# Kernel tuning notes

Measured on AMD Instinct MI355X. Metric: run time of the kernel, lower is better.

The kernel has to match this reference:

```python
import jax, jax.numpy as jnp
import numpy as np

TEMPERATURE = 0.1
NUM_CLASSES = 21
L2_EPS = 1e-12   # torch F.normalize eps
NEG = -1e9       # masking value for invalid (absent-class) logit slots


def setup_inputs() -> dict:
    key = jax.random.key(0)
    k1, k2 = jax.random.split(key)
    features = jax.random.normal(k1, (16, 512, 64, 64), dtype=jnp.float32)
    labels = jax.random.randint(k2, (16, 513, 513), 0, NUM_CLASSES, dtype=jnp.int32)
    return {"features": features, "labels": labels}


def reference(features, labels):
    B, D, H, W = features.shape
    C = NUM_CLASSES
    # torch: F.interpolate(labels.float()[:,None], (H,W), mode='bilinear').squeeze(1).long()
    lab = jax.image.resize(labels.astype(jnp.float32)[:, None], (B, 1, H, W),
                           method="bilinear", antialias=False)
    lab = lab[:, 0].astype(jnp.int32)                     # [B,H,W]

    # per-image, per-class masked feature pooling (segment reduce)
    masks = (lab[:, None, :, :] == jnp.arange(C)[None, :, None, None]).astype(features.dtype)  # [B,C,H,W]
    sums = jnp.einsum('bdhw,bchw->bcd', features, masks)  # [B,C,D]
    norms = jnp.linalg.norm(sums, axis=-1, keepdims=True)
    protos = sums / jnp.maximum(norms, L2_EPS)            # normalized prototypes [B,C,D]
    pres = masks.sum((2, 3)) > 0                          # [B,C] class present in image

    # all pairwise prototype dots: S[c,e,i,j] = <proto[i,c], proto[j,e]> / T
    S = jnp.einsum('icd,jed->ceij', protos, protos) / TEMPERATURE  # [C,C,B,B]
    presT = pres.T                                        # [C,B]
    valid = presT[:, None, :, None] & presT[None, :, None, :]       # [C,C,B,B]
    masked = jnp.where(valid, S, NEG)

    idx = jnp.arange(C)
    diag = masked[idx, idx]                               # [C,B,B] positive block S[c,c]
    dvalid = valid[idx, idx]                              # [C,B,B]

    # logits for class c = concat(p_block, all n_blocks) -> diag block appears twice
    lse_diag = jax.nn.logsumexp(diag, axis=(1, 2))        # [C]
    lse_all = jax.nn.logsumexp(masked, axis=(1, 2, 3))    # [C]
    lse = jnp.logaddexp(lse_diag, lse_all)                # [C]

    cnt = dvalid.sum((1, 2))
    pos_mean = jnp.where(dvalid, diag, 0.0).sum((1, 2)) / jnp.maximum(cnt, 1)

    cls_present = pres.any(0)                             # [C]
    loss = jnp.sum(jnp.where(cls_present, lse - pos_mean, 0.0))
    return loss
```

## Files before the change

kernel.cpp:

```cpp
#include <hip/hip_runtime.h>
#include <cstdint>
#include <cstddef>

#define NUM_C 21
#define NROW 336
#define N2   (NROW * NROW)
#define KSLABS 16

typedef __attribute__((ext_vector_type(8))) short short8;
typedef __attribute__((ext_vector_type(4))) float f32x4;
typedef __attribute__((ext_vector_type(16))) float f32x16;
typedef __attribute__((ext_vector_type(4))) int int4v;

union frag_u { int4v i; short8 s; };
__device__ __forceinline__ short8 mk_frag(uint32_t a0, uint32_t a1, uint32_t a2, uint32_t a3) {
    frag_u u; u.i = int4v{(int)a0, (int)a1, (int)a2, (int)a3}; return u.s;
}
__device__ __forceinline__ uint32_t mask_pair(uint32_t eL, uint32_t eH, uint32_t c) {
    return (eL == c ? 0x3F80u : 0u) | (eH == c ? 0x3F800000u : 0u);
}

__global__ __launch_bounds__(256) void k1_resize_hist(const int* __restrict__ labels,
                                                      uint8_t* __restrict__ lab,
                                                      int* __restrict__ countsPart,
                                                      float* __restrict__ out) {
    int b = blockIdx.x >> 4, strip = blockIdx.x & 15;
    if (blockIdx.x == 0 && threadIdx.x == 0) out[0] = 0.0f;
    __shared__ int hist[NUM_C];
    if (threadIdx.x < NUM_C) hist[threadIdx.x] = 0;
    __syncthreads();

    int p = strip * 256 + threadIdx.x;
    int y = p >> 6, x = p & 63;
    const int* L = labels + (size_t)b * 263169;
    float sy = (y + 0.5f) * 8.015625f - 0.5f;
    float sx = (x + 0.5f) * 8.015625f - 0.5f;
    int y0 = (int)sy; float fy = sy - (float)y0;
    int x0 = (int)sx; float fx = sx - (float)x0;
    const int* r0 = L + y0 * 513 + x0;
    float L00 = (float)__builtin_nontemporal_load(r0);
    float L01 = (float)__builtin_nontemporal_load(r0 + 1);
    float L10 = (float)__builtin_nontemporal_load(r0 + 513);
    float L11 = (float)__builtin_nontemporal_load(r0 + 514);
    float v0 = (1.0f - fx) * L00 + fx * L01;
    float v1 = (1.0f - fx) * L10 + fx * L11;
    float val = (1.0f - fy) * v0 + fy * v1;
    int c = (int)val;
    lab[b * 4096 + p] = (uint8_t)c;
    atomicAdd(&hist[c], 1);
    __syncthreads();
    if (threadIdx.x < NUM_C) countsPart[blockIdx.x * NUM_C + threadIdx.x] = hist[threadIdx.x];
}

__global__ __launch_bounds__(256, 4) void k2_sums(const float* __restrict__ feat,
                                                  const uint8_t* __restrict__ lab,
                                                  float* __restrict__ sums_part) {
    int bid = blockIdx.x;
    int b = bid >> 6, slab = (bid >> 2) & 15, ng = bid & 3;
    int t = threadIdx.x, wv = t >> 6, lane = t & 63;
    int g = lane >> 5;
    int dbase = (ng * 4 + wv) * 32;
    int d = dbase + (lane & 31);
    uint32_t c = lane & 31;
    const float*   fp = feat + ((size_t)(b * 512 + d)) * 4096 + slab * 256 + g * 128;
    const uint8_t* lp = lab + b * 4096 + slab * 256 + g * 128;

    f32x16 acc;
#pragma unroll
    for (int j = 0; j < 16; ++j) acc[j] = 0.0f;

#pragma unroll 4
    for (int s = 0; s < 16; ++s) {
        f32x4 fA = __builtin_nontemporal_load((const f32x4*)(fp + s * 8));
        f32x4 fB = __builtin_nontemporal_load((const f32x4*)(fp + s * 8 + 4));
        uint32_t w0 = *(const uint32_t*)(lp + s * 8);
        uint32_t w1 = *(const uint32_t*)(lp + s * 8 + 4);

        uint32_t u0 = __float_as_uint(fA[0]), u1 = __float_as_uint(fA[1]),
                 u2 = __float_as_uint(fA[2]), u3 = __float_as_uint(fA[3]),
                 u4 = __float_as_uint(fB[0]), u5 = __float_as_uint(fB[1]),
                 u6 = __float_as_uint(fB[2]), u7 = __float_as_uint(fB[3]);
        short8 bHi = mk_frag(__builtin_amdgcn_perm(u1, u0, 0x07060302u),
                             __builtin_amdgcn_perm(u3, u2, 0x07060302u),
                             __builtin_amdgcn_perm(u5, u4, 0x07060302u),
                             __builtin_amdgcn_perm(u7, u6, 0x07060302u));
        float t0 = fA[0] - __uint_as_float(u0 & 0xFFFF0000u);
        float t1 = fA[1] - __uint_as_float(u1 & 0xFFFF0000u);
        float t2 = fA[2] - __uint_as_float(u2 & 0xFFFF0000u);
        float t3 = fA[3] - __uint_as_float(u3 & 0xFFFF0000u);
        float t4 = fB[0] - __uint_as_float(u4 & 0xFFFF0000u);
        float t5 = fB[1] - __uint_as_float(u5 & 0xFFFF0000u);
        float t6 = fB[2] - __uint_as_float(u6 & 0xFFFF0000u);
        float t7 = fB[3] - __uint_as_float(u7 & 0xFFFF0000u);
        short8 bLo = mk_frag(
            __builtin_amdgcn_perm(__float_as_uint(t1), __float_as_uint(t0), 0x07060302u),
            __builtin_amdgcn_perm(__float_as_uint(t3), __float_as_uint(t2), 0x07060302u),
            __builtin_amdgcn_perm(__float_as_uint(t5), __float_as_uint(t4), 0x07060302u),
            __builtin_amdgcn_perm(__float_as_uint(t7), __float_as_uint(t6), 0x07060302u));

        uint32_t e0 = w0 & 255u, e1 = (w0 >> 8) & 255u, e2 = (w0 >> 16) & 255u, e3 = w0 >> 24;
        uint32_t e4 = w1 & 255u, e5 = (w1 >> 8) & 255u, e6 = (w1 >> 16) & 255u, e7 = w1 >> 24;
        short8 a = mk_frag(mask_pair(e0, e1, c), mask_pair(e2, e3, c),
                           mask_pair(e4, e5, c), mask_pair(e6, e7, c));

        acc = __builtin_amdgcn_mfma_f32_32x32x16_bf16(a, bHi, acc, 0, 0, 0);
        acc = __builtin_amdgcn_mfma_f32_32x32x16_bf16(a, bLo, acc, 0, 0, 0);
    }

    float* sp = sums_part + (size_t)slab * NROW * 512;
    int rb = 4 * g;
#pragma unroll
    for (int j = 0; j < 16; ++j) {
        int row = (j & 3) + 8 * (j >> 2) + rb;
        if (row < NUM_C) sp[(size_t)(row * 16 + b) * 512 + d] = acc[j];
    }
}

__global__ __launch_bounds__(256) void k3_fold(const float4* __restrict__ part,
                                               float4* __restrict__ sums) {
    int idx = blockIdx.x * 256 + threadIdx.x;
    float4 s = part[idx];
#pragma unroll
    for (int q = 1; q < KSLABS; ++q) {
        float4 v = part[q * 43008 + idx];
        s.x += v.x; s.y += v.y; s.z += v.z; s.w += v.w;
    }
    sums[idx] = s;
}

__global__ __launch_bounds__(64) void k4_gram(const float* __restrict__ sums,
                                              float* __restrict__ gpart) {
    int row0 = blockIdx.x * 32, col0 = blockIdx.y * 32, k0 = blockIdx.z * 64;
    __shared__ float A[32 * 66], Bt[32 * 66];
    int t = threadIdx.x;
    int row = t >> 1, kk0 = (t & 1) * 32;
#pragma unroll
    for (int q = 0; q < 8; ++q) {
        int kk = kk0 + q * 4;
        int ra = row0 + row, rb = col0 + row;
        float4 va = (ra < NROW) ? *(const float4*)&sums[(size_t)ra * 512 + k0 + kk]
                                : make_float4(0.f, 0.f, 0.f, 0.f);
        float4 vb = (rb < NROW) ? *(const float4*)&sums[(size_t)rb * 512 + k0 + kk]
                                : make_float4(0.f, 0.f, 0.f, 0.f);
        *(float2*)&A[row * 66 + kk]      = make_float2(va.x, va.y);
        *(float2*)&A[row * 66 + kk + 2]  = make_float2(va.z, va.w);
        *(float2*)&Bt[row * 66 + kk]     = make_float2(vb.x, vb.y);
        *(float2*)&Bt[row * 66 + kk + 2] = make_float2(vb.z, vb.w);
    }
    __syncthreads();
    int ty = t >> 3, tx = t & 7;
    float acc[4][4] = {};
    for (int kk = 0; kk < 64; kk += 2) {
        float2 a[4], bb[4];
#pragma unroll
        for (int u = 0; u < 4; ++u) {
            a[u]  = *(const float2*)&A[(ty * 4 + u) * 66 + kk];
            bb[u] = *(const float2*)&Bt[(tx * 4 + u) * 66 + kk];
        }
#pragma unroll
        for (int u = 0; u < 4; ++u)
#pragma unroll
            for (int v = 0; v < 4; ++v)
                acc[u][v] += a[u].x * bb[v].x + a[u].y * bb[v].y;
    }
    float* gp = gpart + (size_t)blockIdx.z * N2;
#pragma unroll
    for (int u = 0; u < 4; ++u) {
        int r1 = row0 + ty * 4 + u;
        if (r1 >= NROW) continue;
        int r2 = col0 + tx * 4;
        if (r2 + 3 < NROW) {
            *(float4*)&gp[(size_t)r1 * NROW + r2] =
                make_float4(acc[u][0], acc[u][1], acc[u][2], acc[u][3]);
        } else {
#pragma unroll
            for (int v = 0; v < 4; ++v)
                if (r2 + v < NROW) gp[(size_t)r1 * NROW + r2 + v] = acc[u][v];
        }
    }
}

__global__ __launch_bounds__(1024) void k5_loss(const float* __restrict__ gpart,
                                                const int* __restrict__ countsPart,
                                                float* __restrict__ out) {
    int c = blockIdx.x, t = threadIdx.x;
    int wv = t >> 6, lane = t & 63;
    __shared__ float invnL[NROW];
    __shared__ uint8_t presL[NROW];
    __shared__ float redE[16], redD[16], redL[16];

    for (int r = t; r < NROW; r += 1024) {
        float ss = 0.0f;
#pragma unroll
        for (int s = 0; s < 8; ++s) ss += gpart[(size_t)s * N2 + (size_t)r * 337];
        invnL[r] = 1.0f / fmaxf(sqrtf(ss), 1e-12f);
        int img = r & 15, cls = r >> 4;
        int cnt = 0;
#pragma unroll
        for (int s = 0; s < 16; ++s) cnt += countsPart[(img * 16 + s) * NUM_C + cls];
        presL[r] = cnt > 0 ? 1 : 0;
    }
    __syncthreads();

    int nc = 0;
#pragma unroll
    for (int j = 0; j < 16; ++j) nc += presL[c * 16 + j];
    if (nc == 0) return;

    float eS = 0.0f, dE = 0.0f, dL = 0.0f;
    for (int idx = t; idx < 16 * NROW; idx += 1024) {
        int i = idx / NROW, r2 = idx - i * NROW;
        int r1 = c * 16 + i;
        float g = 0.0f;
#pragma unroll
        for (int s = 0; s < 8; ++s) g += gpart[(size_t)s * N2 + (size_t)r1 * NROW + r2];
        if (presL[r1] && presL[r2]) {
            float sv = g * invnL[r1] * invnL[r2] * 10.0f;
            float e = expf(sv - 10.0f);
            eS += e;
            if ((r2 >> 4) == c) { dE += e; dL += sv; }
        }
    }
#pragma unroll
    for (int off = 32; off >= 1; off >>= 1) {
        eS += __shfl_xor(eS, off, 64);
        dE += __shfl_xor(dE, off, 64);
        dL += __shfl_xor(dL, off, 64);
    }
    if (lane == 0) { redE[wv] = eS; redD[wv] = dE; redL[wv] = dL; }
    __syncthreads();
    if (t == 0) {
        float E = 0, D = 0, Ln = 0;
#pragma unroll
        for (int w = 0; w < 16; ++w) { E += redE[w]; D += redD[w]; Ln += redL[w]; }
        float lse = 10.0f + logf(E + D);
        float posMean = Ln / (float)(nc * nc);
        atomicAdd(out, lse - posMean);
    }
}

extern "C" void kernel_launch(void* const* d_in, const int* in_sizes, int n_in,
                              void* d_out, int out_size, void* d_ws, size_t ws_size,
                              hipStream_t stream) {
    const float* features = (const float*)d_in[0];
    const int* labels = (const int*)d_in[1];
    char* ws = (char*)d_ws;

    uint8_t* lab     = (uint8_t*)ws;
    int* countsPart  = (int*)(ws + 65536);
    float* sums_part = (float*)(ws + 87040);
    float* sums      = (float*)(ws + 87040 + 11010048);
    float* gpart     = (float*)(ws + 87040 + 11010048 + 688128);
    float* out       = (float*)d_out;

    k1_resize_hist<<<256, 256, 0, stream>>>(labels, lab, countsPart, out);
    k2_sums<<<1024, 256, 0, stream>>>(features, lab, sums_part);
    k3_fold<<<168, 256, 0, stream>>>((const float4*)sums_part, (float4*)sums);
    k4_gram<<<dim3(11, 11, 8), 64, 0, stream>>>(sums, gpart);
    k5_loss<<<21, 1024, 0, stream>>>(gpart, countsPart, out);
}
```

Before: 271.2 us.

## Stage feature rows through LDS with async global_load_lds and restructure k2 tiling

The k2 segment-sum kernel now has each block own 32 feature channels and a quarter of the pixels. Each 256-pixel slab of 32 rows is loaded into shared memory with global_load_lds, so global reads are fully coalesced row segments instead of per-lane strided row reads. Waves then read MFMA fragments from LDS, and each wave writes its own partial slice so the downstream fold still sees 16 partials. This adds barriers and LDS traffic, drops the occupancy hint, and does not double-buffer the loads, so there is no overlap between loading and compute.

New measurement: 217.7 us. 1.25x faster.

```diff
diff --git a/kernel.cpp b/kernel.cpp
--- a/kernel.cpp
+++ b/kernel.cpp
@@ -18,6 +18,10 @@
 }
 __device__ __forceinline__ uint32_t mask_pair(uint32_t eL, uint32_t eH, uint32_t c) {
     return (eL == c ? 0x3F80u : 0u) | (eH == c ? 0x3F800000u : 0u);
+}
+__device__ __forceinline__ void load_lds16(const float* src, float* dst) {
+    __builtin_amdgcn_global_load_lds((const __attribute__((address_space(1))) void*)src,
+                                     (__attribute__((address_space(3))) void*)dst, 16, 0, 2);
 }
 
 __global__ __launch_bounds__(256) void k1_resize_hist(const int* __restrict__ labels,
@@ -52,62 +56,77 @@
     if (threadIdx.x < NUM_C) countsPart[blockIdx.x * NUM_C + threadIdx.x] = hist[threadIdx.x];
 }
 
-__global__ __launch_bounds__(256, 4) void k2_sums(const float* __restrict__ feat,
-                                                  const uint8_t* __restrict__ lab,
-                                                  float* __restrict__ sums_part) {
+__global__ __launch_bounds__(256) void k2_sums(const float* __restrict__ feat,
+                                               const uint8_t* __restrict__ lab,
+                                               float* __restrict__ sums_part) {
     int bid = blockIdx.x;
-    int b = bid >> 6, slab = (bid >> 2) & 15, ng = bid & 3;
+    int b = bid >> 6, dg = (bid >> 2) & 15, ks = bid & 3;
     int t = threadIdx.x, wv = t >> 6, lane = t & 63;
     int g = lane >> 5;
-    int dbase = (ng * 4 + wv) * 32;
-    int d = dbase + (lane & 31);
     uint32_t c = lane & 31;
-    const float*   fp = feat + ((size_t)(b * 512 + d)) * 4096 + slab * 256 + g * 128;
-    const uint8_t* lp = lab + b * 4096 + slab * 256 + g * 128;
+    __shared__ float tile[32 * 260];
+
+    const float* fbase = feat + ((size_t)(b * 512 + dg * 32)) * 4096 + ks * 1024;
+    const uint8_t* lbase = lab + b * 4096 + ks * 1024;
 
     f32x16 acc;
 #pragma unroll
     for (int j = 0; j < 16; ++j) acc[j] = 0.0f;
 
-#pragma unroll 4
-    for (int s = 0; s < 16; ++s) {
-        f32x4 fA = __builtin_nontemporal_load((const f32x4*)(fp + s * 8));
-        f32x4 fB = __builtin_nontemporal_load((const f32x4*)(fp + s * 8 + 4));
-        uint32_t w0 = *(const uint32_t*)(lp + s * 8);
-        uint32_t w1 = *(const uint32_t*)(lp + s * 8 + 4);
-
-        uint32_t u0 = __float_as_uint(fA[0]), u1 = __float_as_uint(fA[1]),
-                 u2 = __float_as_uint(fA[2]), u3 = __float_as_uint(fA[3]),
-                 u4 = __float_as_uint(fB[0]), u5 = __float_as_uint(fB[1]),
-                 u6 = __float_as_uint(fB[2]), u7 = __float_as_uint(fB[3]);
-        short8 bHi = mk_frag(__builtin_amdgcn_perm(u1, u0, 0x07060302u),
-                             __builtin_amdgcn_perm(u3, u2, 0x07060302u),
-                             __builtin_amdgcn_perm(u5, u4, 0x07060302u),
-                             __builtin_amdgcn_perm(u7, u6, 0x07060302u));
-        float t0 = fA[0] - __uint_as_float(u0 & 0xFFFF0000u);
-        float t1 = fA[1] - __uint_as_float(u1 & 0xFFFF0000u);
-        float t2 = fA[2] - __uint_as_float(u2 & 0xFFFF0000u);
-        float t3 = fA[3] - __uint_as_float(u3 & 0xFFFF0000u);
-        float t4 = fB[0] - __uint_as_float(u4 & 0xFFFF0000u);
-        float t5 = fB[1] - __uint_as_float(u5 & 0xFFFF0000u);
-        float t6 = fB[2] - __uint_as_float(u6 & 0xFFFF0000u);
-        float t7 = fB[3] - __uint_as_float(u7 & 0xFFFF0000u);
-        short8 bLo = mk_frag(
-            __builtin_amdgcn_perm(__float_as_uint(t1), __float_as_uint(t0), 0x07060302u),
-            __builtin_amdgcn_perm(__float_as_uint(t3), __float_as_uint(t2), 0x07060302u),
-            __builtin_amdgcn_perm(__float_as_uint(t5), __float_as_uint(t4), 0x07060302u),
-            __builtin_amdgcn_perm(__float_as_uint(t7), __float_as_uint(t6), 0x07060302u));
-
-        uint32_t e0 = w0 & 255u, e1 = (w0 >> 8) & 255u, e2 = (w0 >> 16) & 255u, e3 = w0 >> 24;
-        uint32_t e4 = w1 & 255u, e5 = (w1 >> 8) & 255u, e6 = (w1 >> 16) & 255u, e7 = w1 >> 24;
-        short8 a = mk_frag(mask_pair(e0, e1, c), mask_pair(e2, e3, c),
-                           mask_pair(e4, e5, c), mask_pair(e6, e7, c));
-
-        acc = __builtin_amdgcn_mfma_f32_32x32x16_bf16(a, bHi, acc, 0, 0, 0);
-        acc = __builtin_amdgcn_mfma_f32_32x32x16_bf16(a, bLo, acc, 0, 0, 0);
-    }
-
-    float* sp = sums_part + (size_t)slab * NROW * 512;
+    for (int slab = 0; slab < 4; ++slab) {
+        int px0 = slab * 256;
+#pragma unroll
+        for (int rr = 0; rr < 8; ++rr) {
+            int r = wv * 8 + rr;
+            load_lds16(fbase + (size_t)r * 4096 + px0 + lane * 4, &tile[r * 260]);
+        }
+        __syncthreads();
+
+        const uint8_t* lp = lbase + px0 + wv * 64 + g * 8;
+        const float* lrow = &tile[(lane & 31) * 260 + wv * 64 + g * 8];
+#pragma unroll
+        for (int ch = 0; ch < 4; ++ch) {
+            f32x4 fA = *(const f32x4*)(lrow + ch * 16);
+            f32x4 fB = *(const f32x4*)(lrow + ch * 16 + 4);
+            uint2 wl = *(const uint2*)(lp + ch * 16);
+
+            uint32_t u0 = __float_as_uint(fA[0]), u1 = __float_as_uint(fA[1]),
+                     u2 = __float_as_uint(fA[2]), u3 = __float_as_uint(fA[3]),
+                     u4 = __float_as_uint(fB[0]), u5 = __float_as_uint(fB[1]),
+                     u6 = __float_as_uint(fB[2]), u7 = __float_as_uint(fB[3]);
+            short8 bHi = mk_frag(__builtin_amdgcn_perm(u1, u0, 0x07060302u),
+                                 __builtin_amdgcn_perm(u3, u2, 0x07060302u),
+                                 __builtin_amdgcn_perm(u5, u4, 0x07060302u),
+                                 __builtin_amdgcn_perm(u7, u6, 0x07060302u));
+            float t0 = fA[0] - __uint_as_float(u0 & 0xFFFF0000u);
+            float t1 = fA[1] - __uint_as_float(u1 & 0xFFFF0000u);
+            float t2 = fA[2] - __uint_as_float(u2 & 0xFFFF0000u);
+            float t3 = fA[3] - __uint_as_float(u3 & 0xFFFF0000u);
+            float t4 = fB[0] - __uint_as_float(u4 & 0xFFFF0000u);
+            float t5 = fB[1] - __uint_as_float(u5 & 0xFFFF0000u);
+            float t6 = fB[2] - __uint_as_float(u6 & 0xFFFF0000u);
+            float t7 = fB[3] - __uint_as_float(u7 & 0xFFFF0000u);
+            short8 bLo = mk_frag(
+                __builtin_amdgcn_perm(__float_as_uint(t1), __float_as_uint(t0), 0x07060302u),
+                __builtin_amdgcn_perm(__float_as_uint(t3), __float_as_uint(t2), 0x07060302u),
+                __builtin_amdgcn_perm(__float_as_uint(t5), __float_as_uint(t4), 0x07060302u),
+                __builtin_amdgcn_perm(__float_as_uint(t7), __float_as_uint(t6), 0x07060302u));
+
+            uint32_t e0 = wl.x & 255u, e1 = (wl.x >> 8) & 255u,
+                     e2 = (wl.x >> 16) & 255u, e3 = wl.x >> 24;
+            uint32_t e4 = wl.y & 255u, e5 = (wl.y >> 8) & 255u,
+                     e6 = (wl.y >> 16) & 255u, e7 = wl.y >> 24;
+            short8 a = mk_frag(mask_pair(e0, e1, c), mask_pair(e2, e3, c),
+                               mask_pair(e4, e5, c), mask_pair(e6, e7, c));
+
+            acc = __builtin_amdgcn_mfma_f32_32x32x16_bf16(a, bHi, acc, 0, 0, 0);
+            acc = __builtin_amdgcn_mfma_f32_32x32x16_bf16(a, bLo, acc, 0, 0, 0);
+        }
+        __syncthreads();
+    }
+
+    float* sp = sums_part + (size_t)(ks * 4 + wv) * NROW * 512;
+    int d = dg * 32 + (lane & 31);
     int rb = 4 * g;
 #pragma unroll
     for (int j = 0; j < 16; ++j) {
```
